# Optimization experiments

Measured on AMD Instinct MI355X. Metric: run time of the kernel, lower is better.

## Reference

```python
import jax, jax.numpy as jnp
import numpy as np

NUM_HEADS = 12
HEAD_DIM = 64
HIDDEN = NUM_HEADS * HEAD_DIM
SCALE = 1.0 / float(np.sqrt(HEAD_DIM))


def _split_heads(x):
    # x: [b, d, s, hidden] -> [b, h, d, s, head_dim]  (transpose_for_scores)
    b, d, s, _ = x.shape
    return jnp.transpose(x.reshape(b, d, s, NUM_HEADS, HEAD_DIM), (0, 3, 1, 2, 4))


def _merge_heads(x):
    # [b, h, d, s, e] -> [b, d, s, hidden]  (untranspose_for_scores)
    b, h, d, s, e = x.shape
    return jnp.transpose(x, (0, 2, 3, 1, 4)).reshape(b, d, s, h * e)


def _segment_attention(q, keys, values, masks, num_docs):
    # _cat_forward: broadcast every key/value/mask list entry to num_docs along
    # dim 2, concat along key length, then scaled-dot-product attention.
    b, h = q.shape[0], q.shape[1]
    q = jnp.broadcast_to(q, (b, h, num_docs, q.shape[3], q.shape[4]))
    k = jnp.concatenate([jnp.broadcast_to(t, (b, h, num_docs, t.shape[3], t.shape[4])) for t in keys], axis=3)
    v = jnp.concatenate([jnp.broadcast_to(t, (b, h, num_docs, t.shape[3], t.shape[4])) for t in values], axis=3)
    mask = jnp.concatenate([jnp.broadcast_to(m, (b, 1, num_docs, 1, m.shape[-1])) for m in masks], axis=-1)
    scores = jnp.einsum('bhdqe,bhdke->bhdqk', q, k) * SCALE + mask
    probs = jax.nn.softmax(scores, axis=-1)
    ctx = jnp.einsum('bhdqk,bhdke->bhdqe', probs, v)
    return _merge_heads(ctx)


def setup_inputs() -> dict:
    key = jax.random.key(0)
    ks = jax.random.split(key, 8)
    B, D, Q, S = 2, 16, 32, 512
    inp = {
        'cls': jax.random.normal(ks[0], (B, 1, 1, HIDDEN), jnp.float32),
        'query': jax.random.normal(ks[1], (B, 1, Q, HIDDEN), jnp.float32),
        'doc': jax.random.normal(ks[2], (B, D, S, HIDDEN), jnp.float32),
        'qmask': jnp.zeros((B, 1, 1, 1, Q), jnp.float32),
        'dmask': jnp.zeros((B, 1, D, 1, S), jnp.float32),
        'Wq': jax.random.normal(ks[3], (HIDDEN, HIDDEN), jnp.float32) * 0.02,
        'bq': jnp.zeros((HIDDEN,), jnp.float32),
        'Wk': jax.random.normal(ks[4], (HIDDEN, HIDDEN), jnp.float32) * 0.02,
        'bk': jnp.zeros((HIDDEN,), jnp.float32),
        'Wv': jax.random.normal(ks[5], (HIDDEN, HIDDEN), jnp.float32) * 0.02,
        'bv': jnp.zeros((HIDDEN,), jnp.float32),
    }
    return inp


def reference(cls, query, doc, qmask, dmask, Wq, bq, Wk, bk, Wv, bv):
    num_docs = doc.shape[1]
    b = cls.shape[0]
    # per-segment q/k/v projections + head split
    segs = {}
    for name, hs in (('cls', cls), ('query', query), ('doc', doc)):
        segs[name] = tuple(_split_heads(hs @ W.T + bb) for W, bb in ((Wq, bq), (Wk, bk), (Wv, bv)))
    cmask = jnp.zeros((b, 1, 1, 1, cls.shape[2]), cls.dtype)  # cls token never padded
    masks = {'cls': cmask, 'query': qmask, 'doc': dmask}
    names = ('cls', 'query', 'doc')
    keys = [segs[n][1] for n in names]
    vals = [segs[n][2] for n in names]
    mlist = [masks[n] for n in names]
    # all segment->segment attention flags default True; attention_window_size
    # is None so each segment goes through the _cat_forward path
    outs = [_segment_attention(segs[n][0], keys, vals, mlist, num_docs) for n in names]
    # cls:[b,D,1,H], query:[b,D,Q,H], doc:[b,D,S,H] -> concat along seq for one output
    return jnp.concatenate(outs, axis=2)
```

## Files before the change

### kernel.cpp

```cpp
#include <hip/hip_runtime.h>
#include <hip/hip_bf16.h>

#define NH      12
#define HD      64
#define HID     768
#define B_      2
#define D_      16
#define QL      32
#define SL      512
#define SEQ     545
#define RPB     8225
#define TOT_ROWS 16450
#define PAD_ROWS 16512
#define VT_R    8256
#define WSZ     589824
#define SCALE_  0.125f
#define LOG2E   1.4426950408889634f

typedef __attribute__((ext_vector_type(8))) short short8;
typedef __attribute__((ext_vector_type(4))) short short4v;
typedef __attribute__((ext_vector_type(4))) float float4v;
typedef __attribute__((ext_vector_type(2))) unsigned int uint2v;

__device__ __forceinline__ short f2bf(float f) {
    __hip_bfloat16 h = __float2bfloat16(f);
    short s; __builtin_memcpy(&s, &h, 2);
    return s;
}

__device__ __forceinline__ unsigned int cvtpk(float a, float b) {
    unsigned int r;
    asm("v_cvt_pk_bf16_f32 %0, %1, %2" : "=v"(r) : "v"(a), "v"(b));
    return r;
}

__device__ __forceinline__ void gl2lds16(const short* g, short* l) {
    __builtin_amdgcn_global_load_lds(
        (const __attribute__((address_space(1))) void*)g,
        (__attribute__((address_space(3))) void*)l, 16, 0, 0);
}

__global__ __launch_bounds__(256) void pack_kernel(
    const float* __restrict__ cls, const float* __restrict__ query,
    const float* __restrict__ doc, short* __restrict__ X)
{
    int idx = (blockIdx.x * 256 + threadIdx.x) * 4;
    int row = idx / HID;
    int col = idx - row * HID;
    float4 v = make_float4(0.f, 0.f, 0.f, 0.f);
    if (row < TOT_ROWS) {
        int b = row / RPB;
        int r = row - b * RPB;
        const float* src;
        if (r == 0)        src = cls   + b * HID + col;
        else if (r < 33)   src = query + ((size_t)(b * QL + (r - 1))) * HID + col;
        else               src = doc   + ((size_t)(b * (D_ * SL) + (r - 33))) * HID + col;
        v = *reinterpret_cast<const float4*>(src);
    }
    short4v o;
    o[0] = f2bf(v.x); o[1] = f2bf(v.y); o[2] = f2bf(v.z); o[3] = f2bf(v.w);
    *reinterpret_cast<short4v*>(X + idx) = o;
}

__global__ __launch_bounds__(256) void wpack_kernel(
    const float* __restrict__ Wq, const float* __restrict__ Wk,
    const float* __restrict__ Wv, short* __restrict__ Wb)
{
    int idx = (blockIdx.x * 256 + threadIdx.x) * 4;
    int z = idx / WSZ;
    int r = idx - z * WSZ;
    const float* src = (z == 0 ? Wq : (z == 1 ? Wk : Wv)) + r;
    float4 v = *reinterpret_cast<const float4*>(src);
    short4v o;
    o[0] = f2bf(v.x); o[1] = f2bf(v.y); o[2] = f2bf(v.z); o[3] = f2bf(v.w);
    *reinterpret_cast<short4v*>(Wb + idx) = o;
}

__global__ __launch_bounds__(256) void proj4u(
    const short* __restrict__ X, const short* __restrict__ Wb,
    const float* __restrict__ bq, const float* __restrict__ bk,
    const float* __restrict__ bv,
    short* __restrict__ Qb, short* __restrict__ Kb, short* __restrict__ Vt)
{
    __shared__ short Xs[2][128 * 32];
    __shared__ short Ws[2][128 * 32];

    int tid = threadIdx.x, lane = tid & 63, wave = tid >> 6;

    int lin = blockIdx.x + 18 * blockIdx.y;
    {
        const int q = 290, r = 2;
        int xcd = lin & 7, seq = lin >> 3;
        lin = (xcd < r ? xcd * (q + 1) : r * (q + 1) + (xcd - r) * q) + seq;
    }
    int mblk = lin / 18;
    int nz   = lin - mblk * 18;
    int zi   = nz % 3;
    int nblk = nz / 3;
    bool vsw = (zi == 2);
    const short* W = Wb + (size_t)zi * WSZ;
    int m0 = mblk * 128, n0 = nblk * 128;

    int moff = (wave & 1) * 64, noff = (wave >> 1) * 64;
    int lr = lane & 15, lg = lane >> 4, lk = lg * 8;
    int srow = lane >> 2, sk = (lane & 3) * 8;

    const short* xg0 = X + (size_t)(m0 + wave * 32 + srow) * HID + sk;
    const short* xg1 = xg0 + (size_t)16 * HID;
    const short* wg0 = W + (size_t)(n0 + wave * 32 + srow) * HID + sk;
    const short* wg1 = wg0 + (size_t)16 * HID;

    float4v acc[4][4];
    for (int mi = 0; mi < 4; ++mi)
        for (int ni = 0; ni < 4; ++ni)
            acc[mi][ni] = (float4v){0.f, 0.f, 0.f, 0.f};

#define PSTAGE(bufi, kt) do {                                   \
    gl2lds16(xg0 + (kt) * 32, &Xs[bufi][wave * 1024]);          \
    gl2lds16(xg1 + (kt) * 32, &Xs[bufi][wave * 1024 + 512]);    \
    gl2lds16(wg0 + (kt) * 32, &Ws[bufi][wave * 1024]);          \
    gl2lds16(wg1 + (kt) * 32, &Ws[bufi][wave * 1024 + 512]); } while (0)

    PSTAGE(0, 0);
#pragma unroll
    for (int kt = 0; kt < 24; ++kt) {
        __syncthreads();
        if (kt < 23) PSTAGE((kt + 1) & 1, kt + 1);
        const short* xb = Xs[kt & 1];
        const short* wb = Ws[kt & 1];
        short8 af[4], bf2[4];
        for (int mi = 0; mi < 4; ++mi)
            af[mi]  = *reinterpret_cast<const short8*>(&xb[(moff + mi * 16 + lr) * 32 + lk]);
        for (int ni = 0; ni < 4; ++ni)
            bf2[ni] = *reinterpret_cast<const short8*>(&wb[(noff + ni * 16 + lr) * 32 + lk]);
        if (!vsw) {
            for (int mi = 0; mi < 4; ++mi)
                for (int ni = 0; ni < 4; ++ni)
                    acc[mi][ni] = __builtin_amdgcn_mfma_f32_16x16x32_bf16(
                        af[mi], bf2[ni], acc[mi][ni], 0, 0, 0);
        } else {
            for (int mi = 0; mi < 4; ++mi)
                for (int ni = 0; ni < 4; ++ni)
                    acc[mi][ni] = __builtin_amdgcn_mfma_f32_16x16x32_bf16(
                        bf2[ni], af[mi], acc[mi][ni], 0, 0, 0);
        }
    }
#undef PSTAGE

    if (!vsw) {
        short* Y = zi == 0 ? Qb : Kb;
        const float* bias = zi == 0 ? bq : bk;
        for (int ni = 0; ni < 4; ++ni) {
            int gcol = n0 + noff + ni * 16 + lr;
            float bb = bias[gcol];
            for (int mi = 0; mi < 4; ++mi) {
                int growb = m0 + moff + mi * 16 + lg * 4;
                for (int r = 0; r < 4; ++r)
                    Y[(size_t)(growb + r) * HID + gcol] = f2bf(acc[mi][ni][r] + bb);
            }
        }
    } else {
        for (int ni = 0; ni < 4; ++ni) {
            float4 b4 = *reinterpret_cast<const float4*>(&bv[n0 + noff + ni * 16 + lg * 4]);
            const float* bbr = reinterpret_cast<const float*>(&b4);
            for (int mi = 0; mi < 4; ++mi) {
                int grow = m0 + moff + mi * 16 + lr;
                if (grow >= TOT_ROWS) continue;
                int b  = grow >= RPB ? 1 : 0;
                int rb = grow - b * RPB;
                int vr = rb < 33 ? rb : rb + 7;
                size_t cb = ((size_t)(b * HID + n0 + noff + ni * 16 + lg * 4)) * VT_R;
                for (int r = 0; r < 4; ++r)
                    Vt[cb + (size_t)r * VT_R + vr] = f2bf(acc[mi][ni][r] + bbr[r]);
            }
        }
    }
}

__device__ __forceinline__ int row_of(int b, int d, int t) {
    t = t > 544 ? 544 : t;
    int base = b * RPB;
    if (t < 512)  return base + 33 + d * SL + t;
    if (t == 512) return base;
    return base + (t - 512);
}

__global__ __launch_bounds__(256) void attn4(
    const short* __restrict__ Qb, const short* __restrict__ Kb,
    const short* __restrict__ Vt,
    const float* __restrict__ qmask, const float* __restrict__ dmask,
    float* __restrict__ out)
{
    __shared__ short Ks[2][64 * 64];
    __shared__ short Vs[2][64 * 64];
    __shared__ float maskv[576];

    int tid  = threadIdx.x;
    int lane = tid & 63, wave = tid >> 6;

    int lin = blockIdx.x + 5 * blockIdx.y;
    {
        int xcd = lin & 7, seq = lin >> 3;
        lin = xcd * 240 + seq;
    }
    int hbd = lin / 5;
    int qc  = lin - hbd * 5;
    int h = hbd >> 5, bd = hbd & 31;
    int b = bd >> 4, d = bd & 15;

    int lr = lane & 15, lg = lane >> 4, lk = lg * 8;
    int base = b * RPB;
    const short* vbase = Vt + (size_t)(b * HID + h * HD) * VT_R;

#define ASTAGE(bufi, kt) do {                                               \
    for (int p = 0; p < 2; ++p) {                                           \
        int s2 = p * 256 + tid;                                             \
        int r = s2 >> 3, c = s2 & 7;                                        \
        const short* g = Kb + (size_t)row_of(b, d, (kt) * 64 + r) * HID     \
                       + h * HD + ((c ^ (r & 7)) * 8);                      \
        gl2lds16(g, &Ks[bufi][(p * 256 + (tid & 0xC0)) * 8]);               \
    }                                                                       \
    for (int p = 0; p < 2; ++p) {                                           \
        int s2 = p * 256 + tid;                                             \
        int rd = s2 >> 3, c = s2 & 7;                                       \
        int tc = (kt) * 64 + ((c ^ (rd & 7)) * 8);                          \
        int vr = tc < 512 ? 40 + d * SL + tc : tc - 512;                    \
        gl2lds16(vbase + (size_t)rd * VT_R + vr,                            \
                 &Vs[bufi][(p * 256 + (tid & 0xC0)) * 8]);                  \
    } } while (0)

    ASTAGE(0, 0);

    for (int i = tid; i < 576; i += 256) {
        float mv;
        if (i < 512)       mv = dmask[(size_t)(b * D_ + d) * SL + i];
        else if (i == 512) mv = 0.f;
        else if (i < 545)  mv = qmask[b * QL + (i - 513)];
        else               mv = -INFINITY;
        maskv[i] = mv * LOG2E;
    }

    short8 bq0[2], bq1[2];
    for (int s = 0; s < 2; ++s) {
        int qtok = qc * 128 + s * 64 + wave * 16 + lr;
        int qrow = qtok < 512 ? base + 33 + d * SL + qtok : base + qtok - 512;
        const short* qp = Qb + (size_t)qrow * HID + h * HD + lk;
        bq0[s] = *reinterpret_cast<const short8*>(qp);
        bq1[s] = *reinterpret_cast<const short8*>(qp + 32);
    }

    float m_i[2] = {-1e30f, -1e30f}, l_i[2] = {0.f, 0.f};
    float4v o[2][4];
    for (int s = 0; s < 2; ++s)
        for (int nt = 0; nt < 4; ++nt) o[s][nt] = (float4v){0.f, 0.f, 0.f, 0.f};

    const float qs = SCALE_ * LOG2E;

#pragma unroll
    for (int kt = 0; kt < 9; ++kt) {
        __syncthreads();
        if (kt < 8) ASTAGE((kt + 1) & 1, kt + 1);
        const short* kb = Ks[kt & 1];
        const short* vbuf = Vs[kt & 1];

        short8 kf0[4], kf1[4];
        for (int nt = 0; nt < 4; ++nt) {
            int r = nt * 16 + lr;
            int x0 = lg ^ (r & 7);
            kf0[nt] = *reinterpret_cast<const short8*>(&kb[r * 64 + x0 * 8]);
            kf1[nt] = *reinterpret_cast<const short8*>(&kb[r * 64 + (x0 ^ 4) * 8]);
        }

        for (int s = 0; s < 2; ++s) {
            float p4[4][4];
            __builtin_amdgcn_s_setprio(1);
            for (int nt = 0; nt < 4; ++nt) {
                float4v z = (float4v){0.f, 0.f, 0.f, 0.f};
                z = __builtin_amdgcn_mfma_f32_16x16x32_bf16(kf0[nt], bq0[s], z, 0, 0, 0);
                z = __builtin_amdgcn_mfma_f32_16x16x32_bf16(kf1[nt], bq1[s], z, 0, 0, 0);
                float4v mk = *reinterpret_cast<const float4v*>(
                    &maskv[kt * 64 + nt * 16 + lg * 4]);
                for (int r = 0; r < 4; ++r) p4[nt][r] = z[r] * qs + mk[r];
            }
            __builtin_amdgcn_s_setprio(0);

            float a0 = fmaxf(fmaxf(p4[0][0], p4[0][1]), p4[0][2]);
            float a1 = fmaxf(fmaxf(p4[0][3], p4[1][0]), p4[1][1]);
            float a2 = fmaxf(fmaxf(p4[1][2], p4[1][3]), p4[2][0]);
            float a3 = fmaxf(fmaxf(p4[2][1], p4[2][2]), p4[2][3]);
            float a4 = fmaxf(fmaxf(p4[3][0], p4[3][1]), p4[3][2]);
            float b0 = fmaxf(fmaxf(a0, a1), a2);
            float b1 = fmaxf(fmaxf(a3, a4), p4[3][3]);
            float tmx = fmaxf(b0, b1);
            tmx = fmaxf(tmx, __shfl_xor(tmx, 16));
            tmx = fmaxf(tmx, __shfl_xor(tmx, 32));

            if (__any(tmx > m_i[s] + 8.0f)) {
                float mnew = fmaxf(m_i[s], tmx);
                float alpha = exp2f(m_i[s] - mnew);
                m_i[s] = mnew;
                l_i[s] *= alpha;
                float al[4];
                for (int r = 0; r < 4; ++r) al[r] = __shfl(alpha, lg * 4 + r);
                for (int nt = 0; nt < 4; ++nt)
                    for (int r = 0; r < 4; ++r) o[s][nt][r] *= al[r];
            }

            float sum = 0.f;
            for (int nt = 0; nt < 4; ++nt)
                for (int r = 0; r < 4; ++r) {
                    p4[nt][r] = exp2f(p4[nt][r] - m_i[s]);
                    sum += p4[nt][r];
                }
            sum += __shfl_xor(sum, 16);
            sum += __shfl_xor(sum, 32);
            l_i[s] += sum;

            unsigned int wa[4], wbv[4];
            for (int nt = 0; nt < 4; ++nt) {
                wa[nt]  = cvtpk(p4[nt][0], p4[nt][1]);
                wbv[nt] = cvtpk(p4[nt][2], p4[nt][3]);
            }
            uint2v tA01 = __builtin_amdgcn_permlane32_swap(wa[0],  wa[1],  false, false);
            uint2v uA01 = __builtin_amdgcn_permlane16_swap(tA01[0], tA01[1], false, false);
            uint2v tB01 = __builtin_amdgcn_permlane32_swap(wbv[0], wbv[1], false, false);
            uint2v uB01 = __builtin_amdgcn_permlane16_swap(tB01[0], tB01[1], false, false);
            uint2v tA23 = __builtin_amdgcn_permlane32_swap(wa[2],  wa[3],  false, false);
            uint2v uA23 = __builtin_amdgcn_permlane16_swap(tA23[0], tA23[1], false, false);
            uint2v tB23 = __builtin_amdgcn_permlane32_swap(wbv[2], wbv[3], false, false);
            uint2v uB23 = __builtin_amdgcn_permlane16_swap(tB23[0], tB23[1], false, false);

            union { unsigned int u[4]; short8 s8; } A0, A1;
            A0.u[0] = uA01[0]; A0.u[1] = uB01[0]; A0.u[2] = uA01[1]; A0.u[3] = uB01[1];
            A1.u[0] = uA23[0]; A1.u[1] = uB23[0]; A1.u[2] = uA23[1]; A1.u[3] = uB23[1];
            short8 ap0 = A0.s8;
            short8 ap1 = A1.s8;

            __builtin_amdgcn_s_setprio(1);
            for (int nt = 0; nt < 4; ++nt) {
                int rd = nt * 16 + lr;
                int x0 = lg ^ (rd & 7);
                short8 bv0 = *reinterpret_cast<const short8*>(&vbuf[rd * 64 + x0 * 8]);
                short8 bv1 = *reinterpret_cast<const short8*>(&vbuf[rd * 64 + (x0 ^ 4) * 8]);
                o[s][nt] = __builtin_amdgcn_mfma_f32_16x16x32_bf16(ap0, bv0, o[s][nt], 0, 0, 0);
                o[s][nt] = __builtin_amdgcn_mfma_f32_16x16x32_bf16(ap1, bv1, o[s][nt], 0, 0, 0);
            }
            __builtin_amdgcn_s_setprio(0);
        }
    }
#undef ASTAGE

    for (int s = 0; s < 2; ++s) {
        float li[4];
        for (int r = 0; r < 4; ++r) li[r] = __shfl(l_i[s], lg * 4 + r);
        for (int r = 0; r < 4; ++r) {
            int t = qc * 128 + s * 64 + wave * 16 + lg * 4 + r;
            if (t >= SEQ) continue;
            int seq = t < 512 ? 33 + t : (t == 512 ? 0 : t - 512);
            float inv = 1.f / li[r];
            float* op = out + ((size_t)(bd * SEQ + seq)) * HID + h * HD + lr;
            for (int nt = 0; nt < 4; ++nt)
                op[nt * 16] = o[s][nt][r] * inv;
        }
    }
}

extern "C" void kernel_launch(void* const* d_in, const int* in_sizes, int n_in,
                              void* d_out, int out_size, void* d_ws, size_t ws_size,
                              hipStream_t stream)
{
    const float* cls   = (const float*)d_in[0];
    const float* query = (const float*)d_in[1];
    const float* doc   = (const float*)d_in[2];
    const float* qmask = (const float*)d_in[3];
    const float* dmask = (const float*)d_in[4];
    const float* Wq = (const float*)d_in[5];
    const float* bq = (const float*)d_in[6];
    const float* Wk = (const float*)d_in[7];
    const float* bk = (const float*)d_in[8];
    const float* Wv = (const float*)d_in[9];
    const float* bv = (const float*)d_in[10];
    float* out = (float*)d_out;

    short* X  = (short*)d_ws;
    size_t seg = (size_t)PAD_ROWS * HID;
    short* Qb = X + seg;
    short* Kb = Qb + seg;
    short* Vt = Kb + seg;
    short* Wb = (short*)d_out;

    pack_kernel<<<dim3((PAD_ROWS * HID / 4) / 256), 256, 0, stream>>>(cls, query, doc, X);
    wpack_kernel<<<dim3((3 * WSZ / 4) / 256), 256, 0, stream>>>(Wq, Wk, Wv, Wb);
    proj4u<<<dim3(18, 129, 1), 256, 0, stream>>>(X, Wb, bq, bk, bv, Qb, Kb, Vt);
    attn4<<<dim3(5, NH * 32, 1), 256, 0, stream>>>(Qb, Kb, Vt, qmask, dmask, out);
}
```

Baseline: 312.8 us.

## Fold softmax scale into Wq, merge pack kernels, defer row-sum reductions

Merges the activation and weight bf16 pack kernels into one launch. It pre-multiplies Wq and bq by scale*log2e so the attention kernel can seed the MFMA accumulator with the mask instead of applying a scale-and-add per score. It also keeps per-lane partial row sums and does the cross-lane reduction once at the end, and runs the max shuffles only when a rescale is triggered. Rounding the scaled weights to bf16 changes numerics slightly, and correctness relies on the lane-partial max test being a valid trigger.

```diff
diff --git a/kernel.cpp b/kernel.cpp
--- a/kernel.cpp
+++ b/kernel.cpp
@@ -16,6 +16,7 @@
 #define WSZ     589824
 #define SCALE_  0.125f
 #define LOG2E   1.4426950408889634f
+#define QSF     0.18033688011112042f
 
 typedef __attribute__((ext_vector_type(8))) short short8;
 typedef __attribute__((ext_vector_type(4))) short short4v;
@@ -40,40 +41,46 @@
         (__attribute__((address_space(3))) void*)l, 16, 0, 0);
 }
 
-__global__ __launch_bounds__(256) void pack_kernel(
+#define PACK_BLKS  12384
+#define WPACK_BLKS 1728
+
+__global__ __launch_bounds__(256) void pack_all(
     const float* __restrict__ cls, const float* __restrict__ query,
-    const float* __restrict__ doc, short* __restrict__ X)
+    const float* __restrict__ doc,
+    const float* __restrict__ Wq, const float* __restrict__ Wk,
+    const float* __restrict__ Wv,
+    short* __restrict__ X, short* __restrict__ Wb)
 {
-    int idx = (blockIdx.x * 256 + threadIdx.x) * 4;
-    int row = idx / HID;
-    int col = idx - row * HID;
-    float4 v = make_float4(0.f, 0.f, 0.f, 0.f);
-    if (row < TOT_ROWS) {
-        int b = row / RPB;
-        int r = row - b * RPB;
-        const float* src;
-        if (r == 0)        src = cls   + b * HID + col;
-        else if (r < 33)   src = query + ((size_t)(b * QL + (r - 1))) * HID + col;
-        else               src = doc   + ((size_t)(b * (D_ * SL) + (r - 33))) * HID + col;
-        v = *reinterpret_cast<const float4*>(src);
-    }
-    short4v o;
-    o[0] = f2bf(v.x); o[1] = f2bf(v.y); o[2] = f2bf(v.z); o[3] = f2bf(v.w);
-    *reinterpret_cast<short4v*>(X + idx) = o;
-}
-
-__global__ __launch_bounds__(256) void wpack_kernel(
-    const float* __restrict__ Wq, const float* __restrict__ Wk,
-    const float* __restrict__ Wv, short* __restrict__ Wb)
-{
-    int idx = (blockIdx.x * 256 + threadIdx.x) * 4;
-    int z = idx / WSZ;
-    int r = idx - z * WSZ;
-    const float* src = (z == 0 ? Wq : (z == 1 ? Wk : Wv)) + r;
-    float4 v = *reinterpret_cast<const float4*>(src);
-    short4v o;
-    o[0] = f2bf(v.x); o[1] = f2bf(v.y); o[2] = f2bf(v.z); o[3] = f2bf(v.w);
-    *reinterpret_cast<short4v*>(Wb + idx) = o;
+    int bid = blockIdx.x;
+    if (bid < PACK_BLKS) {
+        int idx = (bid * 256 + threadIdx.x) * 4;
+        int row = idx / HID;
+        int col = idx - row * HID;
+        float4 v = make_float4(0.f, 0.f, 0.f, 0.f);
+        if (row < TOT_ROWS) {
+            int b = row / RPB;
+            int r = row - b * RPB;
+            const float* src;
+            if (r == 0)        src = cls   + b * HID + col;
+            else if (r < 33)   src = query + ((size_t)(b * QL + (r - 1))) * HID + col;
+            else               src = doc   + ((size_t)(b * (D_ * SL) + (r - 33))) * HID + col;
+            v = *reinterpret_cast<const float4*>(src);
+        }
+        short4v o;
+        o[0] = f2bf(v.x); o[1] = f2bf(v.y); o[2] = f2bf(v.z); o[3] = f2bf(v.w);
+        *reinterpret_cast<short4v*>(X + idx) = o;
+    } else {
+        int idx = ((bid - PACK_BLKS) * 256 + threadIdx.x) * 4;
+        int z = idx / WSZ;
+        int r = idx - z * WSZ;
+        const float* src = (z == 0 ? Wq : (z == 1 ? Wk : Wv)) + r;
+        float sc = (z == 0) ? QSF : 1.0f;
+        float4 v = *reinterpret_cast<const float4*>(src);
+        short4v o;
+        o[0] = f2bf(v.x * sc); o[1] = f2bf(v.y * sc);
+        o[2] = f2bf(v.z * sc); o[3] = f2bf(v.w * sc);
+        *reinterpret_cast<short4v*>(Wb + idx) = o;
+    }
 }
 
 __global__ __launch_bounds__(256) void proj4u(
@@ -150,9 +157,10 @@
     if (!vsw) {
         short* Y = zi == 0 ? Qb : Kb;
         const float* bias = zi == 0 ? bq : bk;
+        float bsc = zi == 0 ? QSF : 1.0f;
         for (int ni = 0; ni < 4; ++ni) {
             int gcol = n0 + noff + ni * 16 + lr;
-            float bb = bias[gcol];
+            float bb = bias[gcol] * bsc;
             for (int mi = 0; mi < 4; ++mi) {
                 int growb = m0 + moff + mi * 16 + lg * 4;
                 for (int r = 0; r < 4; ++r)
@@ -249,12 +257,11 @@
         bq1[s] = *reinterpret_cast<const short8*>(qp + 32);
     }
 
-    float m_i[2] = {-1e30f, -1e30f}, l_i[2] = {0.f, 0.f};
+    float m_i[2] = {-1e30f, -1e30f};
+    float lp[2]  = {0.f, 0.f};
     float4v o[2][4];
     for (int s = 0; s < 2; ++s)
         for (int nt = 0; nt < 4; ++nt) o[s][nt] = (float4v){0.f, 0.f, 0.f, 0.f};
-
-    const float qs = SCALE_ * LOG2E;
 
 #pragma unroll
     for (int kt = 0; kt < 9; ++kt) {
@@ -275,46 +282,43 @@
             float p4[4][4];
             __builtin_amdgcn_s_setprio(1);
             for (int nt = 0; nt < 4; ++nt) {
-                float4v z = (float4v){0.f, 0.f, 0.f, 0.f};
+                float4v z = *reinterpret_cast<const float4v*>(
+                    &maskv[kt * 64 + nt * 16 + lg * 4]);
                 z = __builtin_amdgcn_mfma_f32_16x16x32_bf16(kf0[nt], bq0[s], z, 0, 0, 0);
                 z = __builtin_amdgcn_mfma_f32_16x16x32_bf16(kf1[nt], bq1[s], z, 0, 0, 0);
-                float4v mk = *reinterpret_cast<const float4v*>(
-                    &maskv[kt * 64 + nt * 16 + lg * 4]);
-                for (int r = 0; r < 4; ++r) p4[nt][r] = z[r] * qs + mk[r];
+                for (int r = 0; r < 4; ++r) p4[nt][r] = z[r];
             }
             __builtin_amdgcn_s_setprio(0);
 
-            float a0 = fmaxf(fmaxf(p4[0][0], p4[0][1]), p4[0][2]);
-            float a1 = fmaxf(fmaxf(p4[0][3], p4[1][0]), p4[1][1]);
-            float a2 = fmaxf(fmaxf(p4[1][2], p4[1][3]), p4[2][0]);
-            float a3 = fmaxf(fmaxf(p4[2][1], p4[2][2]), p4[2][3]);
-            float a4 = fmaxf(fmaxf(p4[3][0], p4[3][1]), p4[3][2]);
-            float b0 = fmaxf(fmaxf(a0, a1), a2);
-            float b1 = fmaxf(fmaxf(a3, a4), p4[3][3]);
-            float tmx = fmaxf(b0, b1);
-            tmx = fmaxf(tmx, __shfl_xor(tmx, 16));
-            tmx = fmaxf(tmx, __shfl_xor(tmx, 32));
-
-            if (__any(tmx > m_i[s] + 8.0f)) {
+            float c0 = fmaxf(fmaxf(p4[0][0], p4[0][1]), p4[0][2]);
+            float c1 = fmaxf(fmaxf(p4[0][3], p4[1][0]), p4[1][1]);
+            float c2 = fmaxf(fmaxf(p4[1][2], p4[1][3]), p4[2][0]);
+            float c3 = fmaxf(fmaxf(p4[2][1], p4[2][2]), p4[2][3]);
+            float c4 = fmaxf(fmaxf(p4[3][0], p4[3][1]), p4[3][2]);
+            float lmax = fmaxf(fmaxf(fmaxf(c0, c1), fmaxf(c2, c3)),
+                               fmaxf(c4, p4[3][3]));
+
+            if (__any(lmax > m_i[s] + 8.0f)) {
+                float tmx = fmaxf(lmax, __shfl_xor(lmax, 16));
+                tmx = fmaxf(tmx, __shfl_xor(tmx, 32));
                 float mnew = fmaxf(m_i[s], tmx);
                 float alpha = exp2f(m_i[s] - mnew);
                 m_i[s] = mnew;
-                l_i[s] *= alpha;
+                lp[s] *= alpha;
                 float al[4];
                 for (int r = 0; r < 4; ++r) al[r] = __shfl(alpha, lg * 4 + r);
                 for (int nt = 0; nt < 4; ++nt)
                     for (int r = 0; r < 4; ++r) o[s][nt][r] *= al[r];
             }
 
-            float sum = 0.f;
             for (int nt = 0; nt < 4; ++nt)
-                for (int r = 0; r < 4; ++r) {
+                for (int r = 0; r < 4; ++r)
                     p4[nt][r] = exp2f(p4[nt][r] - m_i[s]);
-                    sum += p4[nt][r];
-                }
-            sum += __shfl_xor(sum, 16);
-            sum += __shfl_xor(sum, 32);
-            l_i[s] += sum;
+            float s0 = (p4[0][0] + p4[0][1]) + (p4[0][2] + p4[0][3]);
+            float s1 = (p4[1][0] + p4[1][1]) + (p4[1][2] + p4[1][3]);
+            float s2 = (p4[2][0] + p4[2][1]) + (p4[2][2] + p4[2][3]);
+            float s3 = (p4[3][0] + p4[3][1]) + (p4[3][2] + p4[3][3]);
+            lp[s] += (s0 + s1) + (s2 + s3);
 
             unsigned int wa[4], wbv[4];
             for (int nt = 0; nt < 4; ++nt) {
@@ -351,8 +355,11 @@
 #undef ASTAGE
 
     for (int s = 0; s < 2; ++s) {
+        float lt = lp[s];
+        lt += __shfl_xor(lt, 16);
+        lt += __shfl_xor(lt, 32);
         float li[4];
-        for (int r = 0; r < 4; ++r) li[r] = __shfl(l_i[s], lg * 4 + r);
+        for (int r = 0; r < 4; ++r) li[r] = __shfl(lt, lg * 4 + r);
         for (int r = 0; r < 4; ++r) {
             int t = qc * 128 + s * 64 + wave * 16 + lg * 4 + r;
             if (t >= SEQ) continue;
@@ -389,8 +396,8 @@
     short* Vt = Kb + seg;
     short* Wb = (short*)d_out;
 
-    pack_kernel<<<dim3((PAD_ROWS * HID / 4) / 256), 256, 0, stream>>>(cls, query, doc, X);
-    wpack_kernel<<<dim3((3 * WSZ / 4) / 256), 256, 0, stream>>>(Wq, Wk, Wv, Wb);
+    pack_all<<<dim3(PACK_BLKS + WPACK_BLKS), 256, 0, stream>>>(
+        cls, query, doc, Wq, Wk, Wv, X, Wb);
     proj4u<<<dim3(18, 129, 1), 256, 0, stream>>>(X, Wb, bq, bk, bv, Qb, Kb, Vt);
     attn4<<<dim3(5, NH * 32, 1), 256, 0, stream>>>(Qb, Kb, Vt, qmask, dmask, out);
 }
```

After: 304.2 us. 1.03x faster.
